# Kernel optimization log

Hardware: AMD Instinct MI355X
Metric: run time of the kernel (lower is better)

The kernel has to match this reference:

```python
import jax, jax.numpy as jnp
import numpy as np

EPS = 1e-5

def _batchnorm(x, gamma, beta):
    # BatchNorm1d in training mode: stats over the point (N) dimension, biased var
    mean = x.mean(axis=0)
    var = ((x - mean) ** 2).mean(axis=0)
    return (x - mean) * jax.lax.rsqrt(var + EPS) * gamma + beta

def setup_inputs() -> dict:
    key = jax.random.key(0)
    ks = jax.random.split(key, 6)
    N, C_in, K, B = 262144, 3, 64, 16
    return {
        "feats": jax.random.normal(ks[0], (N, C_in), dtype=jnp.float32),
        "batch_idx": jax.random.randint(ks[1], (N,), 0, B, dtype=jnp.int32),
        "W1": jax.random.normal(ks[2], (128, C_in), dtype=jnp.float32) * 0.1,
        "gamma1": jnp.ones((128,), jnp.float32),
        "beta1": jnp.zeros((128,), jnp.float32),
        "W2": jax.random.normal(ks[3], (64, 256), dtype=jnp.float32) * 0.05,
        "gamma2": jnp.ones((64,), jnp.float32),
        "beta2": jnp.zeros((64,), jnp.float32),
        "W3": jax.random.normal(ks[4], (K, 64), dtype=jnp.float32) * 0.1,
        "b3": jnp.zeros((K,), jnp.float32),
        "num_batches": B,
    }

def reference(feats, batch_idx, W1, gamma1, beta1, W2, gamma2, beta2, W3, b3, num_batches):
    # conv1 (1x1 conv == linear, no bias) + bn1
    x = _batchnorm(feats @ W1.T, gamma1, beta1)          # [N,128]
    # per-batch global max pooling, broadcast back to points
    seg_max = jax.ops.segment_max(x, batch_idx, num_segments=num_batches)  # [B,128]
    x = jnp.concatenate([x, seg_max[batch_idx]], axis=1)  # [N,256]
    # conv2 + bn2 + relu
    x = jax.nn.relu(_batchnorm(x @ W2.T, gamma2, beta2))  # [N,64]
    # conv3 (with bias)
    return x @ W3.T + b3                                   # [N,k]
```

## Files before the change

kernel.cpp:

```cpp
#include <hip/hip_runtime.h>
#include <hip/hip_bf16.h>

#define EPS 1e-5f
#define NPTS 262144
#define NB 16
#define ACBLK 1024

typedef __attribute__((ext_vector_type(8))) short bf16x8;
typedef __attribute__((ext_vector_type(4))) float f32x4;

#define WS_E    0
#define WS_T    192
#define WS_W3   1216
#define WS_MAXF 3264
#define WS_PMOM 5312
#define WS_SCRM 6480
#define WS_SMAX 81232

__device__ inline float decodeu(unsigned u){
  unsigned bits = (u & 0x80000000u) ? (u ^ 0x80000000u) : ~u;
  return __uint_as_float(bits);
}
__device__ inline unsigned f2bf(float f){
  unsigned u = __float_as_uint(f);
  return (u + 0x7FFFu + ((u>>16)&1u)) >> 16;
}
__device__ inline unsigned pack2bf(float lo, float hi){
  return (f2bf(hi)<<16) | (f2bf(lo) & 0xFFFFu);
}
__device__ inline unsigned ordu(float v){
  unsigned bits = __float_as_uint(v);
  return bits ^ (unsigned)(((int)bits>>31) | (int)0x80000000);
}

__global__ __launch_bounds__(256) void kAC(const float* __restrict__ feats,
                                           const int* __restrict__ bidx,
                                           const float* __restrict__ W1,
                                           const float* __restrict__ g1,
                                           float* __restrict__ wsf) {
  __shared__ unsigned lmax[NB*128];
  __shared__ __align__(16) float4 sfeat[256];
  __shared__ float hist[NB*4];
  __shared__ float red[4*9];
  __shared__ unsigned cnt[NB], base[NB];
  int tid = threadIdx.x;
  int lane = tid&63, wv = tid>>6;
  for (int i=tid;i<NB*128;i+=256) lmax[i]=0u;
  if (tid < NB*4) hist[tid]=0.f;
  if (tid < NB) cnt[tid]=0u;
  __syncthreads();
  int p = blockIdx.x*256 + tid;
  float f0=feats[3*p], f1=feats[3*p+1], f2=feats[3*p+2];
  int b = bidx[p];
  atomicAdd(&hist[b*4+0],f0);
  atomicAdd(&hist[b*4+1],f1);
  atomicAdd(&hist[b*4+2],f2);
  atomicAdd(&hist[b*4+3],1.0f);
  unsigned pos = atomicAdd(&cnt[b], 1u);
  { float acc[9]={f0,f1,f2,f0*f0,f0*f1,f0*f2,f1*f1,f1*f2,f2*f2};
    #pragma unroll
    for (int k=0;k<9;k++){
      float v=acc[k];
      v+=__shfl_down(v,32); v+=__shfl_down(v,16); v+=__shfl_down(v,8);
      v+=__shfl_down(v,4);  v+=__shfl_down(v,2);  v+=__shfl_down(v,1);
      if (lane==0) red[wv*9+k]=v;
    }
  }
  __syncthreads();
  if (tid==0){
    unsigned s=0;
    #pragma unroll
    for (int q=0;q<NB;q++){ base[q]=s; s+=cnt[q]; }
  }
  __syncthreads();
  sfeat[base[b]+pos] = make_float4(f0,f1,f2,__int_as_float(b));
  __syncthreads();
  int c0 = lane, c1 = lane+64;
  float sg0 = (g1[c0]>=0.f)?1.f:-1.f;
  float sg1 = (g1[c1]>=0.f)?1.f:-1.f;
  float w00=W1[3*c0]*sg0, w01=W1[3*c0+1]*sg0, w02=W1[3*c0+2]*sg0;
  float w10=W1[3*c1]*sg1, w11=W1[3*c1+1]*sg1, w12=W1[3*c1+2]*sg1;
  const float4* sp = &sfeat[wv*64];
  int bcur = -1; float mm0=0.f, mm1=0.f;
  #pragma unroll 8
  for (int k=0;k<64;k++){
    float4 f = sp[k];
    float v0 = fmaf(f.z,w02,fmaf(f.y,w01,f.x*w00));
    float v1 = fmaf(f.z,w12,fmaf(f.y,w11,f.x*w10));
    int b2 = __builtin_amdgcn_readfirstlane(__float_as_int(f.w));
    if (b2 != bcur){
      if (bcur >= 0){
        atomicMax(&lmax[bcur*128+c0], ordu(mm0));
        atomicMax(&lmax[bcur*128+c1], ordu(mm1));
      }
      bcur = b2; mm0 = v0; mm1 = v1;
    } else {
      mm0 = fmaxf(mm0,v0); mm1 = fmaxf(mm1,v1);
    }
  }
  atomicMax(&lmax[bcur*128+c0], ordu(mm0));
  atomicMax(&lmax[bcur*128+c1], ordu(mm1));
  __syncthreads();
  float* scrM = wsf + WS_SCRM + blockIdx.x*73;
  if (tid<9) scrM[tid]=red[tid]+red[9+tid]+red[18+tid]+red[27+tid];
  if (tid>=64 && tid<128) scrM[9+tid-64]=hist[tid-64];
  unsigned* spo = (unsigned*)wsf + WS_SMAX + (size_t)blockIdx.x*2048;
  for (int i=tid;i<2048;i+=256) __builtin_nontemporal_store(lmax[i], &spo[i]);
}

__global__ __launch_bounds__(512) void kMx(const float* __restrict__ W3,
                                           float* __restrict__ wsf){
  __shared__ unsigned red[16][32];
  __shared__ float mred[2][73];
  int tid = threadIdx.x, blk = blockIdx.x;
  int g = tid >> 5;
  int e = blk*32 + (tid & 31);
  const unsigned* smax = (const unsigned*)wsf + WS_SMAX;
  unsigned m = 0;
  #pragma unroll 8
  for (int k=g*64; k<g*64+64; k++){
    unsigned t = __builtin_nontemporal_load(&smax[(size_t)k*2048 + e]);
    m = t>m ? t : m;
  }
  red[g][tid&31] = m;
  if (blk < 16 && tid < 146){
    int h = (tid >= 73) ? 1 : 0, mm = tid - 73*h;
    float s = 0; const float* sm0 = wsf + WS_SCRM;
    int k0 = blk*64 + h*32;
    #pragma unroll 4
    for (int k=k0; k<k0+32; k++) s += sm0[k*73 + mm];
    mred[h][mm] = s;
  }
  if (blk >= 16 && blk < 18){
    int q = (blk-16)*512 + tid;
    float4 v = ((const float4*)W3)[q];
    unsigned* w3u = (unsigned*)wsf + WS_W3;
    w3u[2*q]   = pack2bf(v.x, v.y);
    w3u[2*q+1] = pack2bf(v.z, v.w);
  }
  __syncthreads();
  if (tid < 32){
    unsigned u = red[0][tid];
    #pragma unroll
    for (int q=1;q<16;q++){ unsigned t=red[q][tid]; u = t>u?t:u; }
    ((unsigned*)wsf)[WS_MAXF + blk*32 + tid] = u;
  }
  if (blk < 16 && tid < 73)
    wsf[WS_PMOM + blk*73 + tid] = mred[0][tid] + mred[1][tid];
}

__global__ __launch_bounds__(128) void kB2(const float* __restrict__ W1,
    const float* __restrict__ g1, const float* __restrict__ b1,
    const float* __restrict__ W2, const float* __restrict__ g2,
    const float* __restrict__ b2, float* __restrict__ wsf){
  __shared__ float smom[80];
  __shared__ float dred[2][20];
  int tid = threadIdx.x, c = blockIdx.x;
  int lane = tid & 63, wv = tid >> 6;
  if (tid < 73){
    float s = 0; const float* pm = wsf + WS_PMOM;
    #pragma unroll
    for (int g=0; g<16; g++) s += pm[g*73 + tid];
    smom[tid] = s;
  }
  int j = tid;
  float w2f = W2[c*256 + j];
  float w2b = W2[c*256 + 128 + j];
  float w10 = W1[3*j], w11 = W1[3*j+1], w12 = W1[3*j+2];
  float g1j = g1[j], b1j = b1[j];
  unsigned um[16];
  { const unsigned* mf = (const unsigned*)wsf + WS_MAXF;
    #pragma unroll
    for (int b=0;b<16;b++) um[b] = mf[b*128 + j];
  }
  __syncthreads();
  const float invN = 1.0f/NPTS;
  float mean = (w10*smom[0]+w11*smom[1]+w12*smom[2])*invN;
  float ex2 = (w10*w10*smom[3]+w11*w11*smom[6]+w12*w12*smom[8]
             + 2.f*(w10*w11*smom[4]+w10*w12*smom[5]+w11*w12*smom[7]))*invN;
  float var = ex2 - mean*mean;
  float sc = g1j*rsqrtf(var+EPS);
  float sh = b1j - mean*sc;
  float asc = fabsf(sc);
  float p[20];
  p[0] = w2f*(sc*w10); p[1] = w2f*(sc*w11); p[2] = w2f*(sc*w12); p[3] = w2f*sh;
  #pragma unroll
  for (int b=0;b<16;b++) p[4+b] = w2b * fmaf(asc, decodeu(um[b]), sh);
  #pragma unroll
  for (int k=0;k<20;k++){
    float v = p[k];
    v+=__shfl_down(v,32); v+=__shfl_down(v,16); v+=__shfl_down(v,8);
    v+=__shfl_down(v,4);  v+=__shfl_down(v,2);  v+=__shfl_down(v,1);
    if (lane==0) dred[wv][k] = v;
  }
  __syncthreads();
  if (tid == 0){
    float fin[20];
    #pragma unroll
    for (int k=0;k<20;k++) fin[k] = dred[0][k] + dred[1][k];
    float e0=fin[0], e1=fin[1], e2=fin[2], gc=fin[3];
    float sumY = e0*smom[0]+e1*smom[1]+e2*smom[2];
    float sumYY = e0*e0*smom[3]+e1*e1*smom[6]+e2*e2*smom[8]
               + 2.f*(e0*e1*smom[4]+e0*e2*smom[5]+e1*e2*smom[7]);
    float hbs[16];
    #pragma unroll
    for (int b=0;b<16;b++){
      float nb = smom[9+b*4+3];
      float hb = gc + fin[4+b];
      hbs[b] = hb;
      float eS1b = e0*smom[9+b*4]+e1*smom[9+b*4+1]+e2*smom[9+b*4+2];
      sumY += nb*hb;
      sumYY += 2.f*hb*eS1b + nb*hb*hb;
    }
    float mean2 = sumY*invN;
    float var2 = sumYY*invN - mean2*mean2;
    float s2 = g2[c]*rsqrtf(var2+EPS);
    float t2 = b2[c] - mean2*s2;
    wsf[WS_E + c]      = e0*s2;
    wsf[WS_E + 64 + c] = e1*s2;
    wsf[WS_E + 128 + c]= e2*s2;
    #pragma unroll
    for (int b=0;b<16;b++) wsf[WS_T + b*64 + c] = hbs[b]*s2 + t2;
  }
}

__global__ __launch_bounds__(256, 4) void kF(const float* __restrict__ feats,
                                             const int* __restrict__ bidx,
                                             const float* __restrict__ wsf,
                                             const float* __restrict__ b3,
                                             float* __restrict__ out) {
  __shared__ __align__(16) unsigned char SB[36992];
  unsigned* zbuf = (unsigned*)SB;
  float* Tl = (float*)(SB + 32768);
  float* fbuf = (float*)SB;
  int tid = threadIdx.x;
  for (int i=tid;i<NB*64;i+=256) Tl[(i>>6)*66 + (i&63)] = wsf[WS_T + i];
  int lane = tid & 63, wv = tid >> 6;
  int col = lane & 15, kgrp = lane >> 4;
  const ushort* w3b = (const ushort*)((const unsigned*)wsf + WS_W3);
  bf16x8 bfr[4][2];
  #pragma unroll
  for (int n=0;n<4;n++)
    #pragma unroll
    for (int kk=0;kk<2;kk++)
      bfr[n][kk] = *(const bf16x8*)(w3b + (n*16+col)*64 + kk*32 + kgrp*8);
  float bias[4];
  #pragma unroll
  for (int n=0;n<4;n++) bias[n] = b3[n*16+col];
  __syncthreads();
  const float* Eg = wsf + WS_E;
  int p0 = (blockIdx.x*4 + wv)*64;
  int p = p0 + lane;
  float f0 = feats[3*p], f1 = feats[3*p+1], f2 = feats[3*p+2];
  int b = bidx[p];
  const float* tb = &Tl[b*66];
  unsigned rowbase = (unsigned)(wv*64+lane)*32;
  unsigned sw = (lane&7)<<2;
  #pragma unroll
  for (int j=0;j<8;j++){
    unsigned w[4];
    #pragma unroll
    for (int q=0;q<4;q++){
      int c = j*8 + q*2;
      float2 tp = *(const float2*)(tb + c);
      float y0 = fmaf(Eg[c],  f0, fmaf(Eg[64+c],  f1, fmaf(Eg[128+c],  f2, tp.x)));
      float y1 = fmaf(Eg[c+1],f0, fmaf(Eg[64+c+1],f1, fmaf(Eg[128+c+1],f2, tp.y)));
      w[q] = pack2bf(fmaxf(y0,0.f), fmaxf(y1,0.f));
    }
    uint4 ch; ch.x=w[0]; ch.y=w[1]; ch.z=w[2]; ch.w=w[3];
    *(uint4*)&zbuf[rowbase + (((unsigned)(j*4)) ^ sw)] = ch;
  }
  __syncthreads();
  bf16x8 af[4][2];
  #pragma unroll
  for (int m=0;m<4;m++){
    int row = m*16 + col;
    unsigned rb = (unsigned)(wv*64+row)*32;
    unsigned sw2 = (unsigned)(row&7)<<2;
    #pragma unroll
    for (int kk=0;kk<2;kk++){
      unsigned off = ((unsigned)(kk*16 + kgrp*4)) ^ sw2;
      af[m][kk] = *(const bf16x8*)&zbuf[rb + off];
    }
  }
  __syncthreads();
  #pragma unroll
  for (int half=0; half<2; half++){
    f32x4 acc[2][4];
    #pragma unroll
    for (int mi=0;mi<2;mi++)
      #pragma unroll
      for (int n=0;n<4;n++)
        acc[mi][n] = (f32x4){0.f,0.f,0.f,0.f};
    #pragma unroll
    for (int kk=0;kk<2;kk++)
      #pragma unroll
      for (int mi=0;mi<2;mi++)
        #pragma unroll
        for (int n=0;n<4;n++)
          acc[mi][n] = __builtin_amdgcn_mfma_f32_16x16x32_bf16(af[half*2+mi][kk], bfr[n][kk], acc[mi][n], 0,0,0);
    #pragma unroll
    for (int mi=0;mi<2;mi++){
      #pragma unroll
      for (int n=0;n<4;n++){
        #pragma unroll
        for (int r=0;r<4;r++)
          fbuf[wv*2176 + (mi*16 + kgrp*4 + r)*68 + n*16 + col] = acc[mi][n][r] + bias[n];
      }
    }
    __syncthreads();
    #pragma unroll
    for (int it=0; it<8; it++){
      int idx = it*256 + tid;
      int gr = idx >> 4;
      int c4 = (idx & 15) * 4;
      f32x4 v = *(const f32x4*)&fbuf[(gr>>5)*2176 + (gr&31)*68 + c4];
      int orow = blockIdx.x*256 + (gr>>5)*64 + half*32 + (gr&31);
      __builtin_nontemporal_store(v, (f32x4*)&out[(size_t)orow*64 + c4]);
    }
    __syncthreads();
  }
}

extern "C" void kernel_launch(void* const* d_in, const int* in_sizes, int n_in,
                              void* d_out, int out_size, void* d_ws, size_t ws_size,
                              hipStream_t stream) {
  const float* feats = (const float*)d_in[0];
  const int*   bidx  = (const int*)d_in[1];
  const float* W1 = (const float*)d_in[2];
  const float* g1 = (const float*)d_in[3];
  const float* b1 = (const float*)d_in[4];
  const float* W2 = (const float*)d_in[5];
  const float* g2 = (const float*)d_in[6];
  const float* b2 = (const float*)d_in[7];
  const float* W3 = (const float*)d_in[8];
  const float* b3 = (const float*)d_in[9];
  float* wsf = (float*)d_ws;
  float* out = (float*)d_out;
  kAC<<<ACBLK, 256, 0, stream>>>(feats, bidx, W1, g1, wsf);
  kMx<<<64, 512, 0, stream>>>(W3, wsf);
  kB2<<<64, 128, 0, stream>>>(W1, g1, b1, W2, g2, b2, wsf);
  kF<<<ACBLK, 256, 0, stream>>>(feats, bidx, wsf, b3, out);
}
```

Baseline: 62.67 us.

## Enlarge stats blocks to halve partials, stage E in LDS, parallelize kB2 tail

The first pass now uses 512-thread blocks over 512 points each. That halves the number of per-block max/moment partials the reduction kernel must scan, and the partial stores and loads become regular rather than nontemporal. kB2 stages the partial moments in LDS and spreads the per-batch tail over 16 threads instead of one. kF copies the E coefficients into LDS and reads them as float2 instead of from global memory. These changes aim to cut reduction traffic and serial latency in the small kernels, at the cost of larger per-block LDS use and more barriers.

```diff
diff --git a/kernel.cpp b/kernel.cpp
--- a/kernel.cpp
+++ b/kernel.cpp
@@ -4,7 +4,6 @@
 #define EPS 1e-5f
 #define NPTS 262144
 #define NB 16
-#define ACBLK 1024
 
 typedef __attribute__((ext_vector_type(8))) short bf16x8;
 typedef __attribute__((ext_vector_type(4))) float f32x4;
@@ -15,7 +14,7 @@
 #define WS_MAXF 3264
 #define WS_PMOM 5312
 #define WS_SCRM 6480
-#define WS_SMAX 81232
+#define WS_SMAX 43856
 
 __device__ inline float decodeu(unsigned u){
   unsigned bits = (u & 0x80000000u) ? (u ^ 0x80000000u) : ~u;
@@ -33,23 +32,23 @@
   return bits ^ (unsigned)(((int)bits>>31) | (int)0x80000000);
 }
 
-__global__ __launch_bounds__(256) void kAC(const float* __restrict__ feats,
+__global__ __launch_bounds__(512) void kAC(const float* __restrict__ feats,
                                            const int* __restrict__ bidx,
                                            const float* __restrict__ W1,
                                            const float* __restrict__ g1,
                                            float* __restrict__ wsf) {
   __shared__ unsigned lmax[NB*128];
-  __shared__ __align__(16) float4 sfeat[256];
+  __shared__ __align__(16) float4 sfeat[512];
   __shared__ float hist[NB*4];
-  __shared__ float red[4*9];
+  __shared__ float red[8*9];
   __shared__ unsigned cnt[NB], base[NB];
   int tid = threadIdx.x;
   int lane = tid&63, wv = tid>>6;
-  for (int i=tid;i<NB*128;i+=256) lmax[i]=0u;
+  for (int i=tid;i<NB*128;i+=512) lmax[i]=0u;
   if (tid < NB*4) hist[tid]=0.f;
   if (tid < NB) cnt[tid]=0u;
   __syncthreads();
-  int p = blockIdx.x*256 + tid;
+  int p = blockIdx.x*512 + tid;
   float f0=feats[3*p], f1=feats[3*p+1], f2=feats[3*p+2];
   int b = bidx[p];
   atomicAdd(&hist[b*4+0],f0);
@@ -102,10 +101,15 @@
   atomicMax(&lmax[bcur*128+c1], ordu(mm1));
   __syncthreads();
   float* scrM = wsf + WS_SCRM + blockIdx.x*73;
-  if (tid<9) scrM[tid]=red[tid]+red[9+tid]+red[18+tid]+red[27+tid];
+  if (tid<9){
+    float s=0;
+    #pragma unroll
+    for (int q=0;q<8;q++) s += red[q*9+tid];
+    scrM[tid]=s;
+  }
   if (tid>=64 && tid<128) scrM[9+tid-64]=hist[tid-64];
   unsigned* spo = (unsigned*)wsf + WS_SMAX + (size_t)blockIdx.x*2048;
-  for (int i=tid;i<2048;i+=256) __builtin_nontemporal_store(lmax[i], &spo[i]);
+  for (int i=tid;i<2048;i+=512) spo[i]=lmax[i];
 }
 
 __global__ __launch_bounds__(512) void kMx(const float* __restrict__ W3,
@@ -118,17 +122,17 @@
   const unsigned* smax = (const unsigned*)wsf + WS_SMAX;
   unsigned m = 0;
   #pragma unroll 8
-  for (int k=g*64; k<g*64+64; k++){
-    unsigned t = __builtin_nontemporal_load(&smax[(size_t)k*2048 + e]);
+  for (int k=g*32; k<g*32+32; k++){
+    unsigned t = smax[(size_t)k*2048 + e];
     m = t>m ? t : m;
   }
   red[g][tid&31] = m;
   if (blk < 16 && tid < 146){
     int h = (tid >= 73) ? 1 : 0, mm = tid - 73*h;
     float s = 0; const float* sm0 = wsf + WS_SCRM;
-    int k0 = blk*64 + h*32;
+    int k0 = blk*32 + h*16;
     #pragma unroll 4
-    for (int k=k0; k<k0+32; k++) s += sm0[k*73 + mm];
+    for (int k=k0; k<k0+16; k++) s += sm0[k*73 + mm];
     mred[h][mm] = s;
   }
   if (blk >= 16 && blk < 18){
@@ -153,16 +157,15 @@
     const float* __restrict__ g1, const float* __restrict__ b1,
     const float* __restrict__ W2, const float* __restrict__ g2,
     const float* __restrict__ b2, float* __restrict__ wsf){
+  __shared__ float spm[16*73];
   __shared__ float smom[80];
   __shared__ float dred[2][20];
+  __shared__ float sfin[20];
+  __shared__ float pY[16], pYY[16], hbs[16];
+  __shared__ float s2t2[2];
   int tid = threadIdx.x, c = blockIdx.x;
   int lane = tid & 63, wv = tid >> 6;
-  if (tid < 73){
-    float s = 0; const float* pm = wsf + WS_PMOM;
-    #pragma unroll
-    for (int g=0; g<16; g++) s += pm[g*73 + tid];
-    smom[tid] = s;
-  }
+  for (int i=tid;i<16*73;i+=128) spm[i] = wsf[WS_PMOM + i];
   int j = tid;
   float w2f = W2[c*256 + j];
   float w2b = W2[c*256 + 128 + j];
@@ -172,6 +175,13 @@
   { const unsigned* mf = (const unsigned*)wsf + WS_MAXF;
     #pragma unroll
     for (int b=0;b<16;b++) um[b] = mf[b*128 + j];
+  }
+  __syncthreads();
+  if (tid < 73){
+    float s = 0;
+    #pragma unroll
+    for (int g=0; g<16; g++) s += spm[g*73 + tid];
+    smom[tid] = s;
   }
   __syncthreads();
   const float invN = 1.0f/NPTS;
@@ -194,24 +204,24 @@
     if (lane==0) dred[wv][k] = v;
   }
   __syncthreads();
+  if (tid < 20) sfin[tid] = dred[0][tid] + dred[1][tid];
+  __syncthreads();
+  if (tid < 16){
+    int b = tid;
+    float e0=sfin[0],e1=sfin[1],e2=sfin[2],gc=sfin[3];
+    float nb = smom[9+b*4+3];
+    float hb = gc + sfin[4+b];
+    float eS1b = e0*smom[9+b*4]+e1*smom[9+b*4+1]+e2*smom[9+b*4+2];
+    hbs[b]=hb; pY[b]=nb*hb; pYY[b]=2.f*hb*eS1b+nb*hb*hb;
+  }
+  __syncthreads();
   if (tid == 0){
-    float fin[20];
-    #pragma unroll
-    for (int k=0;k<20;k++) fin[k] = dred[0][k] + dred[1][k];
-    float e0=fin[0], e1=fin[1], e2=fin[2], gc=fin[3];
+    float e0=sfin[0],e1=sfin[1],e2=sfin[2];
     float sumY = e0*smom[0]+e1*smom[1]+e2*smom[2];
     float sumYY = e0*e0*smom[3]+e1*e1*smom[6]+e2*e2*smom[8]
                + 2.f*(e0*e1*smom[4]+e0*e2*smom[5]+e1*e2*smom[7]);
-    float hbs[16];
-    #pragma unroll
-    for (int b=0;b<16;b++){
-      float nb = smom[9+b*4+3];
-      float hb = gc + fin[4+b];
-      hbs[b] = hb;
-      float eS1b = e0*smom[9+b*4]+e1*smom[9+b*4+1]+e2*smom[9+b*4+2];
-      sumY += nb*hb;
-      sumYY += 2.f*hb*eS1b + nb*hb*hb;
-    }
+    #pragma unroll
+    for (int b=0;b<16;b++){ sumY += pY[b]; sumYY += pYY[b]; }
     float mean2 = sumY*invN;
     float var2 = sumYY*invN - mean2*mean2;
     float s2 = g2[c]*rsqrtf(var2+EPS);
@@ -219,9 +229,10 @@
     wsf[WS_E + c]      = e0*s2;
     wsf[WS_E + 64 + c] = e1*s2;
     wsf[WS_E + 128 + c]= e2*s2;
-    #pragma unroll
-    for (int b=0;b<16;b++) wsf[WS_T + b*64 + c] = hbs[b]*s2 + t2;
-  }
+    s2t2[0]=s2; s2t2[1]=t2;
+  }
+  __syncthreads();
+  if (tid < 16) wsf[WS_T + tid*64 + c] = hbs[tid]*s2t2[0] + s2t2[1];
 }
 
 __global__ __launch_bounds__(256, 4) void kF(const float* __restrict__ feats,
@@ -229,12 +240,14 @@
                                              const float* __restrict__ wsf,
                                              const float* __restrict__ b3,
                                              float* __restrict__ out) {
-  __shared__ __align__(16) unsigned char SB[36992];
+  __shared__ __align__(16) unsigned char SB[37760];
   unsigned* zbuf = (unsigned*)SB;
   float* Tl = (float*)(SB + 32768);
+  float* sEg = (float*)(SB + 36992);
   float* fbuf = (float*)SB;
   int tid = threadIdx.x;
   for (int i=tid;i<NB*64;i+=256) Tl[(i>>6)*66 + (i&63)] = wsf[WS_T + i];
+  if (tid < 192) sEg[tid] = wsf[WS_E + tid];
   int lane = tid & 63, wv = tid >> 6;
   int col = lane & 15, kgrp = lane >> 4;
   const ushort* w3b = (const ushort*)((const unsigned*)wsf + WS_W3);
@@ -248,7 +261,6 @@
   #pragma unroll
   for (int n=0;n<4;n++) bias[n] = b3[n*16+col];
   __syncthreads();
-  const float* Eg = wsf + WS_E;
   int p0 = (blockIdx.x*4 + wv)*64;
   int p = p0 + lane;
   float f0 = feats[3*p], f1 = feats[3*p+1], f2 = feats[3*p+2];
@@ -262,9 +274,12 @@
     #pragma unroll
     for (int q=0;q<4;q++){
       int c = j*8 + q*2;
-      float2 tp = *(const float2*)(tb + c);
-      float y0 = fmaf(Eg[c],  f0, fmaf(Eg[64+c],  f1, fmaf(Eg[128+c],  f2, tp.x)));
-      float y1 = fmaf(Eg[c+1],f0, fmaf(Eg[64+c+1],f1, fmaf(Eg[128+c+1],f2, tp.y)));
+      float2 e0p = *(const float2*)(sEg + c);
+      float2 e1p = *(const float2*)(sEg + 64 + c);
+      float2 e2p = *(const float2*)(sEg + 128 + c);
+      float2 tp  = *(const float2*)(tb + c);
+      float y0 = fmaf(e0p.x,f0, fmaf(e1p.x,f1, fmaf(e2p.x,f2, tp.x)));
+      float y1 = fmaf(e0p.y,f0, fmaf(e1p.y,f1, fmaf(e2p.y,f2, tp.y)));
       w[q] = pack2bf(fmaxf(y0,0.f), fmaxf(y1,0.f));
     }
     uint4 ch; ch.x=w[0]; ch.y=w[1]; ch.z=w[2]; ch.w=w[3];
@@ -337,8 +352,8 @@
   const float* b3 = (const float*)d_in[9];
   float* wsf = (float*)d_ws;
   float* out = (float*)d_out;
-  kAC<<<ACBLK, 256, 0, stream>>>(feats, bidx, W1, g1, wsf);
+  kAC<<<512, 512, 0, stream>>>(feats, bidx, W1, g1, wsf);
   kMx<<<64, 512, 0, stream>>>(W3, wsf);
   kB2<<<64, 128, 0, stream>>>(W1, g1, b1, W2, g2, b2, wsf);
-  kF<<<ACBLK, 256, 0, stream>>>(feats, bidx, wsf, b3, out);
-}
+  kF<<<1024, 256, 0, stream>>>(feats, bidx, wsf, b3, out);
+}
```

Result: faster. 54.81 us (-12.5%).
